# Performance work log

Measured on AMD Instinct MI355X. Metric: run time of the kernel, lower is better.

Reference implementation:

```python
import jax, jax.numpy as jnp
import numpy as np

B, L, D, NH, V, T, CYC = 16, 512, 512, 8, 8000, 17, 2
HD = D // NH


def _attn(q, kv, qw, qb, kw, kb, vw, vb, ow, ob):
    # q: [N, Lq, D], kv: [N, Lk, D]; weights stored [in, out] (= torch W.T)
    N, Lq, _ = q.shape
    Lk = kv.shape[1]
    Q = (q @ qw + qb).reshape(N, Lq, NH, HD)
    K = (kv @ kw + kb).reshape(N, Lk, NH, HD)
    Vv = (kv @ vw + vb).reshape(N, Lk, NH, HD)
    scores = jnp.einsum('nqhd,nkhd->nhqk', Q, K) / np.float32(np.sqrt(HD))
    probs = jax.nn.softmax(scores, axis=-1)
    ctx = jnp.einsum('nhqk,nkhd->nqhd', probs, Vv).reshape(N, Lq, D)
    return ctx @ ow + ob


def _ln(x, w, b, eps=1e-12):
    u = x.mean(-1, keepdims=True)
    s = ((x - u) ** 2).mean(-1, keepdims=True)
    return w * (x - u) / jnp.sqrt(s + eps) + b


def setup_inputs() -> dict:
    key = jax.random.key(0)
    ks = jax.random.split(key, 32)
    p = {}
    p['tokens'] = jax.random.randint(ks[0], (B, L, 1), 0, V)
    p['masks'] = jnp.ones((B, L), dtype=jnp.int64)
    p['heads'] = jax.random.randint(ks[1], (B, L), 0, 2)
    p['tails'] = jax.random.randint(ks[2], (B, L), 0, 2)
    p['char_emb'] = jax.random.normal(ks[3], (V, D), jnp.float32) * 0.02
    i = 4
    for pre in ('sat', 'rel'):
        for nm in ('q', 'k', 'v', 'o'):
            p[f'{pre}_{nm}w'] = jax.random.normal(ks[i], (D, D), jnp.float32) * 0.02
            p[f'{pre}_{nm}b'] = jnp.zeros((D,), jnp.float32)
            i += 1
    p['ln_sat_w'] = jnp.ones((D,), jnp.float32)
    p['ln_sat_b'] = jnp.zeros((D,), jnp.float32)
    p['ln_rel_w'] = jnp.ones((D,), jnp.float32)
    p['ln_rel_b'] = jnp.zeros((D,), jnp.float32)
    p['ofc_w'] = jax.random.normal(ks[i], (D, T), jnp.float32) * 0.02
    p['ofc_b'] = jnp.zeros((T,), jnp.float32)
    return p


def reference(tokens, masks, heads, tails, char_emb,
              sat_qw, sat_qb, sat_kw, sat_kb, sat_vw, sat_vb, sat_ow, sat_ob,
              rel_qw, rel_qb, rel_kw, rel_kb, rel_vw, rel_vb, rel_ow, rel_ob,
              ln_sat_w, ln_sat_b, ln_rel_w, ln_rel_b, ofc_w, ofc_b):
    e = char_emb[tokens[:, :, 0]]  # [B, L, D]
    h = e
    s = e.mean(axis=1)  # relay token [B, D] (avg_pool2d over seq)
    for _ in range(CYC):
        # backward cycle_shift in the source is a correct roll-by-(-1)
        h_last = jnp.roll(h, -1, axis=1)
        # forward cycle_shift in the source is sequential in-place: result[:,0]=h[:,-1],
        # result[:,i>=1]=h[:,0] (the write at i=0 propagates). Reproduced faithfully.
        h_next = jnp.concatenate(
            [h[:, -1:, :], jnp.broadcast_to(h[:, :1, :], (B, L - 1, D))], axis=1)
        sm = jnp.broadcast_to(s[:, None, :], (B, L, D))
        c = jnp.stack([h_last, h, h_next, e, sm], axis=2).reshape(B * L, 5, D)
        hq = h.reshape(B * L, 1, D)
        a = _attn(hq, c, sat_qw, sat_qb, sat_kw, sat_kb, sat_vw, sat_vb, sat_ow, sat_ob)
        h = _ln(jax.nn.relu(a), ln_sat_w, ln_sat_b).reshape(B, L, D)
        mc = jnp.concatenate([s[:, None, :], h], axis=1)  # [B, L+1, D]
        r = _attn(s[:, None, :], mc, rel_qw, rel_qb, rel_kw, rel_kb, rel_vw, rel_vb, rel_ow, rel_ob)
        s = _ln(jax.nn.relu(r), ln_rel_w, ln_rel_b)[:, 0, :]
    logits = h @ ofc_w + ofc_b  # [B, L, T]
    return logits
```

## Files before the change

### kernel.cpp

```cpp
#include <hip/hip_runtime.h>
#include <hip/hip_bf16.h>

typedef __hip_bfloat16 bf16;

#define BB 16
#define LL 512
#define DD 512
#define NHH 8
#define HDD 64
#define TT 17
#define MM (BB*LL)
#define RCH 8
#define RCK 65

typedef __attribute__((ext_vector_type(8))) short bfrag;
typedef __attribute__((ext_vector_type(4))) float ffrag;
typedef __attribute__((ext_vector_type(8))) unsigned short us8;

struct Params {
  const int* tokens;
  const float* emb;
  const float *sat_qw, *sat_qb, *sat_kw, *sat_kb, *sat_vw, *sat_vb, *sat_ow, *sat_ob;
  const float *rel_qw, *rel_qb, *rel_kw, *rel_kb, *rel_vw, *rel_vb, *rel_ow, *rel_ob;
  const float *ln_sat_w, *ln_sat_b, *ln_rel_w, *ln_rel_b, *ofc_w, *ofc_b;
  bf16 *ebf, *qkv, *kvbuf, *KeVe, *qbuf, *ctxbf, *WtAll, *WtO, *WtLog;
  float *s, *KsVs, *qr, *Ksr, *Vsr, *mpart, *pws, *out;
};

static __device__ __forceinline__ void gld16(const void* g, void* l){
  __builtin_amdgcn_global_load_lds((const __attribute__((address_space(1))) void*)g,
                                   (__attribute__((address_space(3))) void*)l, 16, 0, 0);
}
static __device__ __forceinline__ float us2f(unsigned short u){
  unsigned int v = ((unsigned int)u) << 16;
  float f; __builtin_memcpy(&f, &v, 4); return f;
}
static __device__ __forceinline__ float hsum8(float v){
  v += __shfl_xor(v, 1); v += __shfl_xor(v, 2); v += __shfl_xor(v, 4);
  return v;
}

__global__ __launch_bounds__(256) void k_init(Params P){
  __shared__ __align__(16) char sm[8192];
  int u = blockIdx.x, t = threadIdx.x;
  if (u < 256){
    int* toks = (int*)sm;
    int b = u >> 4, lc = u & 15;
    if (t < 32) toks[t] = P.tokens[b*LL + lc*32 + t];
    __syncthreads();
    bf16* eb = P.ebf + ((size_t)b*LL + lc*32)*DD;
    for (int d = t; d < DD; d += 256){
      float acc = 0.f;
      #pragma unroll 4
      for (int l = 0; l < 32; l++){
        float v = P.emb[(size_t)toks[l]*DD + d];
        eb[(size_t)l*DD + d] = __float2bfloat16(v);
        acc += v;
      }
      P.mpart[(size_t)u*DD + d] = acc;
    }
    return;
  }
  int w = u - 256;
  int z = w >> 8, xy = w & 255;
  int tx = t & 31, ty = t >> 5;
  if (z == 6){
    int i = (xy << 8) + t;
    int row = i >> 9, k = i & 511;
    P.WtLog[i] = __float2bfloat16(row < TT ? P.ofc_w[(size_t)k*TT + row] : 0.f);
    return;
  }
  float (*tile)[33] = (float(*)[33])sm;
  const float* in = (z==0)?P.sat_qw:(z==1)?P.sat_kw:(z==2)?P.sat_vw:
                    (z==3)?P.rel_kw:(z==4)?P.rel_vw:P.sat_ow;
  bf16* out = (z<5) ? (P.WtAll + (size_t)z*512*512) : P.WtO;
  int bx = (xy & 15)*32, by = (xy >> 4)*32;
  #pragma unroll
  for (int j = 0; j < 32; j += 8)
    tile[ty + j][tx] = in[(size_t)(by + ty + j)*DD + bx + tx];
  __syncthreads();
  #pragma unroll
  for (int j = 0; j < 32; j += 8)
    out[(size_t)(bx + ty + j)*DD + by + tx] = __float2bfloat16(tile[tx][ty + j]);
}

__global__ __launch_bounds__(256) void k_mean2(Params P){
  int i = blockIdx.x*256 + threadIdx.x;
  int b = i >> 9, d = i & 511;
  float acc = 0.f;
  #pragma unroll
  for (int c = 0; c < 16; c++) acc += P.mpart[(size_t)(b*16 + c)*DD + d];
  P.s[i] = acc * (1.0f/LL);
}

__global__ __launch_bounds__(256)
void k_sproj(Params P,
             const float* W0, const float* W1, const float* W2, const float* W3,
             const float* W4,
             const float* bias0, const float* bias1, const float* bias2,
             const float* bias3, const float* bias4,
             float* O0, float* O1, float* O2, float* O3, float* O4,
             int ldc0, int ldc1, int ldc2, int ldc3, int ldc4){
  __shared__ float part[8][32][17];
  const float* A = P.s;
  int t = threadIdx.x;
  int n = t & 31, kg = t >> 5;
  int wi = blockIdx.x >> 4, ch = blockIdx.x & 15;
  const float* W  = (wi==0)?W0:(wi==1)?W1:(wi==2)?W2:(wi==3)?W3:W4;
  const float* bs = (wi==0)?bias0:(wi==1)?bias1:(wi==2)?bias2:(wi==3)?bias3:bias4;
  float* O  = (wi==0)?O0:(wi==1)?O1:(wi==2)?O2:(wi==3)?O3:O4;
  int ldc   = (wi==0)?ldc0:(wi==1)?ldc1:(wi==2)?ldc2:(wi==3)?ldc3:ldc4;
  int col = ch*32 + n;
  float acc[16];
  #pragma unroll
  for (int m = 0; m < 16; m++) acc[m] = 0.f;
  const float* Wp = W + (size_t)(kg*64)*512 + col;
  const float* Ap = A + kg*64;
  for (int k = 0; k < 64; k++){
    float w = Wp[(size_t)k*512];
    #pragma unroll
    for (int m = 0; m < 16; m++) acc[m] = fmaf(Ap[m*512 + k], w, acc[m]);
  }
  #pragma unroll
  for (int m = 0; m < 16; m++) part[kg][n][m] = acc[m];
  __syncthreads();
  for (int o = t; o < 512; o += 256){
    int m = o >> 5, nn = o & 31;
    float v = 0.f;
    #pragma unroll
    for (int g = 0; g < 8; g++) v += part[g][nn][m];
    O[(size_t)m*ldc + ch*32 + nn] = v + bs[ch*32 + nn];
  }
}

__global__ __launch_bounds__(256)
void k_gemm(Params P, const bf16* __restrict__ A, const bf16* __restrict__ Wt,
            const float* b0, const float* b1, const float* b2, const float* b3,
            const float* b4,
            bf16* D0, int ld0, bf16* D1, int ld1, int split){
  const int K = 512;
  __shared__ bf16 As[128*32];
  __shared__ bf16 Bs[128*32];
  int t = threadIdx.x;
  int wave = t >> 6, lane = t & 63;
  int id = blockIdx.x;
  int bm = (((id & 7) << 3) | ((id >> 3) & 7)) * 128;
  int bn = (id >> 6) * 128;
  int wm = (wave & 1) * 64, wn = (wave >> 1) * 64;
  ffrag acc[4][4];
  #pragma unroll
  for (int i = 0; i < 4; i++)
    #pragma unroll
    for (int j = 0; j < 4; j++) acc[i][j] = (ffrag){0.f,0.f,0.f,0.f};

  int srow = t >> 2;
  int scol = ((((t & 3) - ((t >> 3) & 3)) & 3)) * 8;
  const bf16* gA = A  + (size_t)(bm + srow)*K + scol;
  const bf16* gB = Wt + (size_t)(bn + srow)*K + scol;
  char* lA = (char*)As + 16*t;
  char* lB = (char*)Bs + 16*t;
  int q = lane >> 4, r = lane & 15;
  int cs = (((q + (r >> 1)) & 3)) * 8;

  for (int k0 = 0; k0 < K; k0 += 32){
    gld16(gA + k0,          lA);
    gld16(gA + 64*K + k0,   lA + 4096);
    gld16(gB + k0,          lB);
    gld16(gB + 64*K + k0,   lB + 4096);
    __syncthreads();
    bfrag af[4], bfv[4];
    #pragma unroll
    for (int i = 0; i < 4; i++){
      af[i]  = *(const bfrag*)(As + (wm + i*16 + r)*32 + cs);
      bfv[i] = *(const bfrag*)(Bs + (wn + i*16 + r)*32 + cs);
    }
    #pragma unroll
    for (int i = 0; i < 4; i++)
      #pragma unroll
      for (int j = 0; j < 4; j++)
        acc[i][j] = __builtin_amdgcn_mfma_f32_16x16x32_bf16(af[i], bfv[j], acc[i][j], 0, 0, 0);
    __syncthreads();
  }
  #pragma unroll
  for (int i = 0; i < 4; i++){
    #pragma unroll
    for (int j = 0; j < 4; j++){
      int row = bm + wm + i*16 + q*4;
      int col = bn + wn + j*16 + r;
      const float* bp = (col < 512) ? b0 : (col < 1024) ? b1 :
                        (col < 1536) ? b2 : (col < 2048) ? b3 : b4;
      float bias = bp[col & 511];
      bf16* D; int ld;
      if (col < split){ D = D0 + (size_t)row*ld0 + col;         ld = ld0; }
      else            { D = D1 + (size_t)row*ld1 + (col-split); ld = ld1; }
      #pragma unroll
      for (int g = 0; g < 4; g++)
        D[(size_t)g*ld] = __float2bfloat16(acc[i][j][g] + bias);
    }
  }
}

__global__ __launch_bounds__(256) void k_logits(Params P){
  const int K = 512;
  __shared__ bf16 As[128*32];
  __shared__ bf16 Bs[128*32];
  int t = threadIdx.x;
  int wave = t >> 6, lane = t & 63;
  int bm = blockIdx.x * 128;
  int wm = (wave & 1) * 64, wn = (wave >> 1) * 64;
  ffrag acc[4][2];
  #pragma unroll
  for (int i = 0; i < 4; i++){ acc[i][0] = (ffrag){0,0,0,0}; acc[i][1] = (ffrag){0,0,0,0}; }
  int srow = t >> 2;
  int scol = ((((t & 3) - ((t >> 3) & 3)) & 3)) * 8;
  const bf16* gA = P.ebf + (size_t)(bm + srow)*K + scol;
  const bf16* gB = P.WtLog + (size_t)srow*K + scol;
  char* lA = (char*)As + 16*t;
  char* lB = (char*)Bs + 16*t;
  int q = lane >> 4, r = lane & 15;
  int cs = (((q + (r >> 1)) & 3)) * 8;

  for (int k0 = 0; k0 < K; k0 += 32){
    gld16(gA + k0,          lA);
    gld16(gA + 64*K + k0,   lA + 4096);
    gld16(gB + k0,          lB);
    gld16(gB + 64*K + k0,   lB + 4096);
    __syncthreads();
    if (wn == 0){
      bfrag bf0 = *(const bfrag*)(Bs + (r)*32 + cs);
      bfrag bf1 = *(const bfrag*)(Bs + (16 + r)*32 + cs);
      #pragma unroll
      for (int i = 0; i < 4; i++){
        bfrag af = *(const bfrag*)(As + (wm + i*16 + r)*32 + cs);
        acc[i][0] = __builtin_amdgcn_mfma_f32_16x16x32_bf16(af, bf0, acc[i][0], 0, 0, 0);
        acc[i][1] = __builtin_amdgcn_mfma_f32_16x16x32_bf16(af, bf1, acc[i][1], 0, 0, 0);
      }
    }
    __syncthreads();
  }
  if (wn == 0){
    #pragma unroll
    for (int i = 0; i < 4; i++)
      #pragma unroll
      for (int j = 0; j < 2; j++){
        int row = bm + wm + i*16 + q*4;
        int col = j*16 + r;
        if (col < TT){
          float bv = P.ofc_b[col];
          #pragma unroll
          for (int g = 0; g < 4; g++)
            P.out[(size_t)(row + g)*TT + col] = acc[i][j][g] + bv;
        }
      }
  }
}

__global__ __launch_bounds__(256)
void k_sat(Params P, const bf16* qp, int sq, const bf16* kp, const bf16* vp, int skv){
  int tok = blockIdx.x*4 + (threadIdx.x >> 6);
  int l = threadIdx.x & 63;
  int b = tok >> 9, li = tok & 511;
  int off = l*8;
  int t0 = (b << 9) | ((li + 1) & 511);
  int t2 = (b << 9) | (li == 0 ? 511 : 0);
  float qf[8];
  { us8 q8 = *(const us8*)(qp + (size_t)tok*sq + off);
    #pragma unroll
    for (int g = 0; g < 8; g++) qf[g] = us2f(q8[g]); }
  float sc[5];
  int rows[3] = {t0, tok, t2};
  #pragma unroll
  for (int j = 0; j < 3; j++){
    us8 k8 = *(const us8*)(kp + (size_t)rows[j]*skv + off);
    float a = 0.f;
    #pragma unroll
    for (int g = 0; g < 8; g++) a += qf[g]*us2f(k8[g]);
    sc[j] = hsum8(a) * 0.125f;
  }
  { us8 k8 = *(const us8*)(P.KeVe + (size_t)tok*1024 + off);
    float a = 0.f;
    #pragma unroll
    for (int g = 0; g < 8; g++) a += qf[g]*us2f(k8[g]);
    sc[3] = hsum8(a) * 0.125f; }
  { const float* ks = P.KsVs + (size_t)b*1024 + off;
    float4 f0 = *(const float4*)ks, f1 = *(const float4*)(ks + 4);
    float a = qf[0]*f0.x + qf[1]*f0.y + qf[2]*f0.z + qf[3]*f0.w
            + qf[4]*f1.x + qf[5]*f1.y + qf[6]*f1.z + qf[7]*f1.w;
    sc[4] = hsum8(a) * 0.125f; }
  float m = fmaxf(fmaxf(fmaxf(sc[0],sc[1]), fmaxf(sc[2],sc[3])), sc[4]);
  float pr[5], den = 0.f;
  #pragma unroll
  for (int j = 0; j < 5; j++){ pr[j] = __expf(sc[j]-m); den += pr[j]; }
  float inv = 1.0f/den;
  float o[8];
  #pragma unroll
  for (int g = 0; g < 8; g++) o[g] = 0.f;
  #pragma unroll
  for (int j = 0; j < 3; j++){
    us8 v8 = *(const us8*)(vp + (size_t)rows[j]*skv + off);
    #pragma unroll
    for (int g = 0; g < 8; g++) o[g] += pr[j]*us2f(v8[g]);
  }
  { us8 v8 = *(const us8*)(P.KeVe + (size_t)tok*1024 + 512 + off);
    #pragma unroll
    for (int g = 0; g < 8; g++) o[g] += pr[3]*us2f(v8[g]); }
  { const float* vs = P.KsVs + (size_t)b*1024 + 512 + off;
    float4 f0 = *(const float4*)vs, f1 = *(const float4*)(vs + 4);
    o[0] += pr[4]*f0.x; o[1] += pr[4]*f0.y; o[2] += pr[4]*f0.z; o[3] += pr[4]*f0.w;
    o[4] += pr[4]*f1.x; o[5] += pr[4]*f1.y; o[6] += pr[4]*f1.z; o[7] += pr[4]*f1.w; }
  bf16 ob[8];
  #pragma unroll
  for (int g = 0; g < 8; g++) ob[g] = __float2bfloat16(o[g]*inv);
  *(us8*)(P.ctxbf + (size_t)tok*DD + off) = *(const us8*)ob;
}

__global__ __launch_bounds__(256) void k_ln(Params P, const bf16* X, bf16* Y){
  int row = blockIdx.x*4 + (threadIdx.x >> 6);
  int lane = threadIdx.x & 63;
  int off = lane*8;
  us8 x8 = *(const us8*)(X + (size_t)row*DD + off);
  float v[8], sum = 0.f;
  #pragma unroll
  for (int g = 0; g < 8; g++){ v[g] = fmaxf(us2f(x8[g]), 0.f); sum += v[g]; }
  #pragma unroll
  for (int o = 32; o; o >>= 1) sum += __shfl_xor(sum, o);
  float u = sum * (1.0f/DD);
  float d[8], var = 0.f;
  #pragma unroll
  for (int g = 0; g < 8; g++){ d[g] = v[g] - u; var += d[g]*d[g]; }
  #pragma unroll
  for (int o = 32; o; o >>= 1) var += __shfl_xor(var, o);
  float inv = rsqrtf(var * (1.0f/DD) + 1e-12f);
  bf16 ob[8];
  #pragma unroll
  for (int g = 0; g < 8; g++)
    ob[g] = __float2bfloat16(P.ln_sat_w[off+g]*d[g]*inv + P.ln_sat_b[off+g]);
  *(us8*)(Y + (size_t)row*DD + off) = *(const us8*)ob;
}

__global__ __launch_bounds__(256) void k_relp(Params P){
  __shared__ __align__(16) char sm[4096];
  int u = blockIdx.x, t = threadIdx.x;
  int ch = u & 7, hh = (u >> 3) & 7, b = u >> 6;
  float* qs   = (float*)sm;
  float* sc   = (float*)(sm + 256);
  float* red  = (float*)(sm + 1024);
  float (*part)[64] = (float(*)[64])(sm + 2048);
  int base = hh * HDD;
  int j0 = ch * RCK;
  int nk = min(513 - j0, RCK);
  if (t < 64) qs[t] = P.qr[(size_t)b*DD + base + t];
  __syncthreads();
  if (t < nk){
    int j = j0 + t;
    float a = 0.f;
    if (j == 0){
      const float* kr = P.Ksr + (size_t)b*DD + base;
      #pragma unroll
      for (int d = 0; d < 64; d += 4){
        float4 k4 = *(const float4*)(kr + d);
        float4 q4 = *(const float4*)(qs + d);
        a += q4.x*k4.x + q4.y*k4.y + q4.z*k4.z + q4.w*k4.w;
      }
    } else {
      const bf16* kr = P.kvbuf + ((size_t)b*LL + j - 1)*1024 + base;
      #pragma unroll
      for (int d = 0; d < 64; d += 8){
        us8 k8 = *(const us8*)(kr + d);
        #pragma unroll
        for (int g = 0; g < 8; g++) a += qs[d+g] * us2f(k8[g]);
      }
    }
    sc[t] = a * 0.125f;
  }
  __syncthreads();
  red[t] = (t < nk) ? sc[t] : -1e30f; __syncthreads();
  for (int st = 128; st; st >>= 1){ if (t < st) red[t] = fmaxf(red[t], red[t+st]); __syncthreads(); }
  float m = red[0]; __syncthreads();
  if (t < nk) sc[t] = __expf(sc[t] - m);
  __syncthreads();
  red[t] = (t < nk) ? sc[t] : 0.f; __syncthreads();
  for (int st = 128; st; st >>= 1){ if (t < st) red[t] += red[t+st]; __syncthreads(); }
  float l = red[0];
  int d = t & 63, c2 = t >> 6;
  float a = 0.f;
  for (int j = c2; j < nk; j += 4){
    int gj = j0 + j;
    float vv = (gj == 0) ? P.Vsr[(size_t)b*DD + base + d]
                         : __bfloat162float(P.kvbuf[((size_t)b*LL + gj - 1)*1024 + 512 + base + d]);
    a += sc[j] * vv;
  }
  part[c2][d] = a; __syncthreads();
  float* o = P.pws + (((size_t)(b*NHH + hh))*RCH + ch) * 66;
  if (t < 64) o[t] = part[0][t] + part[1][t] + part[2][t] + part[3][t];
  else if (t == 64) o[64] = m;
  else if (t == 65) o[65] = l;
}

__global__ __launch_bounds__(256) void k_reltail(Params P){
  __shared__ __align__(16) char sm[4096];
  int b = blockIdx.x, t = threadIdx.x;
  float* crs = (float*)sm;
  float* red = (float*)(sm + 2048);
  for (int o = t; o < 512; o += 256){
    int hh = o >> 6, d = o & 63;
    const float* p = P.pws + ((size_t)(b*NHH + hh))*RCH*66;
    float M = -1e30f;
    #pragma unroll
    for (int c = 0; c < RCH; c++) M = fmaxf(M, p[c*66 + 64]);
    float den = 0.f, acc = 0.f;
    #pragma unroll
    for (int c = 0; c < RCH; c++){
      float w = __expf(p[c*66 + 64] - M);
      den += w * p[c*66 + 65];
      acc += w * p[c*66 + d];
    }
    crs[o] = acc / den;
  }
  __syncthreads();
  int n0 = t, n1 = t + 256;
  float a0 = P.rel_ob[n0], a1 = P.rel_ob[n1];
  for (int k = 0; k < 512; k++){
    float c = crs[k];
    a0 = fmaf(c, P.rel_ow[(size_t)k*512 + n0], a0);
    a1 = fmaf(c, P.rel_ow[(size_t)k*512 + n1], a1);
  }
  float v0 = fmaxf(a0, 0.f), v1 = fmaxf(a1, 0.f);
  red[t] = v0 + v1; __syncthreads();
  for (int st = 128; st; st >>= 1){ if (t < st) red[t] += red[t+st]; __syncthreads(); }
  float u = red[0] * (1.0f/DD); __syncthreads();
  float d0 = v0 - u, d1 = v1 - u;
  red[t] = d0*d0 + d1*d1; __syncthreads();
  for (int st = 128; st; st >>= 1){ if (t < st) red[t] += red[t+st]; __syncthreads(); }
  float inv = rsqrtf(red[0] * (1.0f/DD) + 1e-12f);
  P.s[(size_t)b*DD + n0] = P.ln_rel_w[n0]*d0*inv + P.ln_rel_b[n0];
  P.s[(size_t)b*DD + n1] = P.ln_rel_w[n1]*d1*inv + P.ln_rel_b[n1];
}

extern "C" void kernel_launch(void* const* d_in, const int* in_sizes, int n_in,
                              void* d_out, int out_size, void* d_ws, size_t ws_size,
                              hipStream_t stream) {
  Params P;
  P.tokens  = (const int*)  d_in[0];
  P.emb     = (const float*)d_in[4];
  P.sat_qw  = (const float*)d_in[5];  P.sat_qb = (const float*)d_in[6];
  P.sat_kw  = (const float*)d_in[7];  P.sat_kb = (const float*)d_in[8];
  P.sat_vw  = (const float*)d_in[9];  P.sat_vb = (const float*)d_in[10];
  P.sat_ow  = (const float*)d_in[11]; P.sat_ob = (const float*)d_in[12];
  P.rel_qw  = (const float*)d_in[13]; P.rel_qb = (const float*)d_in[14];
  P.rel_kw  = (const float*)d_in[15]; P.rel_kb = (const float*)d_in[16];
  P.rel_vw  = (const float*)d_in[17]; P.rel_vb = (const float*)d_in[18];
  P.rel_ow  = (const float*)d_in[19]; P.rel_ob = (const float*)d_in[20];
  P.ln_sat_w= (const float*)d_in[21]; P.ln_sat_b= (const float*)d_in[22];
  P.ln_rel_w= (const float*)d_in[23]; P.ln_rel_b= (const float*)d_in[24];
  P.ofc_w   = (const float*)d_in[25]; P.ofc_b  = (const float*)d_in[26];

  char* p = (char*)d_ws;
  auto alloc = [&](size_t bytes) -> char* {
    char* r = p; p += (bytes + 255) & ~(size_t)255; return r;
  };
  const size_t BIGH = (size_t)MM*DD*2;
  P.ebf   = (bf16*) alloc(BIGH);
  P.qkv   = (bf16*) alloc(3*BIGH);
  P.kvbuf = (bf16*) alloc(2*BIGH);
  P.KeVe  = (bf16*) alloc(2*BIGH);
  P.qbuf  = (bf16*) alloc(BIGH);
  P.ctxbf = (bf16*) alloc(BIGH);
  P.WtAll = (bf16*) alloc((size_t)2560*512*2);
  P.WtO   = (bf16*) alloc((size_t)512*512*2);
  P.WtLog = (bf16*) alloc((size_t)128*512*2);
  P.s     = (float*)alloc(BB*DD*4);
  P.KsVs  = (float*)alloc(BB*1024*4);
  P.qr    = (float*)alloc(BB*DD*4);
  P.Ksr   = (float*)alloc(BB*DD*4);
  P.Vsr   = (float*)alloc(BB*DD*4);
  P.mpart = (float*)alloc((size_t)256*DD*4);
  P.pws   = (float*)alloc((size_t)BB*NHH*RCH*66*4);
  P.out   = (float*)d_out;

  bf16* hbf  = P.ebf;
  bf16* aout = P.qkv;

  k_init<<<2048, 256, 0, stream>>>(P);
  k_mean2<<<32, 256, 0, stream>>>(P);
  k_sproj<<<80, 256, 0, stream>>>(P,
      P.sat_kw, P.sat_vw, P.rel_qw, P.rel_kw, P.rel_vw,
      P.sat_kb, P.sat_vb, P.rel_qb, P.rel_kb, P.rel_vb,
      P.KsVs, P.KsVs + 512, P.qr, P.Ksr, P.Vsr,
      1024, 1024, 512, 512, 512);
  k_gemm<<<768, 256, 0, stream>>>(P, P.ebf, P.WtAll,
      P.sat_qb, P.sat_kb, P.sat_vb, P.sat_vb, P.sat_vb, P.qbuf, 512, P.KeVe, 1024, 512);
  k_sat<<<MM/4, 256, 0, stream>>>(P, P.qbuf, 512, P.KeVe, P.KeVe + 512, 1024);
  k_gemm<<<256, 256, 0, stream>>>(P, P.ctxbf, P.WtO,
      P.sat_ob, P.sat_ob, P.sat_ob, P.sat_ob, P.sat_ob, aout, 512, aout, 512, 512);
  k_ln<<<MM/4, 256, 0, stream>>>(P, aout, hbf);
  k_gemm<<<1280, 256, 0, stream>>>(P, hbf, P.WtAll,
      P.sat_qb, P.sat_kb, P.sat_vb, P.rel_kb, P.rel_vb, P.qkv, 1536, P.kvbuf, 1024, 1536);
  k_relp<<<BB*NHH*RCH, 256, 0, stream>>>(P);
  k_reltail<<<BB, 256, 0, stream>>>(P);
  k_sproj<<<32, 256, 0, stream>>>(P,
      P.sat_kw, P.sat_vw, P.sat_vw, P.sat_vw, P.sat_vw,
      P.sat_kb, P.sat_vb, P.sat_vb, P.sat_vb, P.sat_vb,
      P.KsVs, P.KsVs + 512, P.Vsr, P.Vsr, P.Vsr,
      1024, 1024, 512, 512, 512);
  k_sat<<<MM/4, 256, 0, stream>>>(P, P.qkv, 1536, P.qkv + 512, P.qkv + 1024, 1536);
  k_gemm<<<256, 256, 0, stream>>>(P, P.ctxbf, P.WtO,
      P.sat_ob, P.sat_ob, P.sat_ob, P.sat_ob, P.sat_ob, aout, 512, aout, 512, 512);
  k_ln<<<MM/4, 256, 0, stream>>>(P, aout, hbf);
  k_logits<<<64, 256, 0, stream>>>(P);
}
```

Baseline: 335.3 us.

## Merge sproj into QKV gemm launch and split reltail across more blocks

```diff
diff --git a/kernel.cpp b/kernel.cpp
--- a/kernel.cpp
+++ b/kernel.cpp
@@ -93,19 +93,15 @@
   P.s[i] = acc * (1.0f/LL);
 }
 
-__global__ __launch_bounds__(256)
-void k_sproj(Params P,
-             const float* W0, const float* W1, const float* W2, const float* W3,
-             const float* W4,
-             const float* bias0, const float* bias1, const float* bias2,
-             const float* bias3, const float* bias4,
-             float* O0, float* O1, float* O2, float* O3, float* O4,
-             int ldc0, int ldc1, int ldc2, int ldc3, int ldc4){
-  __shared__ float part[8][32][17];
-  const float* A = P.s;
-  int t = threadIdx.x;
+static __device__ void sproj_unit(int u, int t, char* sm, const float* A,
+    const float* W0, const float* W1, const float* W2, const float* W3, const float* W4,
+    const float* bias0, const float* bias1, const float* bias2, const float* bias3,
+    const float* bias4,
+    float* O0, float* O1, float* O2, float* O3, float* O4,
+    int ldc0, int ldc1, int ldc2, int ldc3, int ldc4){
+  float (*part)[32][17] = (float(*)[32][17])sm;
   int n = t & 31, kg = t >> 5;
-  int wi = blockIdx.x >> 4, ch = blockIdx.x & 15;
+  int wi = u >> 4, ch = u & 15;
   const float* W  = (wi==0)?W0:(wi==1)?W1:(wi==2)?W2:(wi==3)?W3:W4;
   const float* bs = (wi==0)?bias0:(wi==1)?bias1:(wi==2)?bias2:(wi==3)?bias3:bias4;
   float* O  = (wi==0)?O0:(wi==1)?O1:(wi==2)?O2:(wi==3)?O3:O4;
@@ -133,17 +129,14 @@
   }
 }
 
-__global__ __launch_bounds__(256)
-void k_gemm(Params P, const bf16* __restrict__ A, const bf16* __restrict__ Wt,
-            const float* b0, const float* b1, const float* b2, const float* b3,
-            const float* b4,
-            bf16* D0, int ld0, bf16* D1, int ld1, int split){
+static __device__ void gemm_unit(int id, int t, char* sm,
+    const bf16* __restrict__ A, const bf16* __restrict__ Wt,
+    const float* b0, const float* b1, const float* b2, const float* b3, const float* b4,
+    bf16* D0, int ld0, bf16* D1, int ld1, int split){
   const int K = 512;
-  __shared__ bf16 As[128*32];
-  __shared__ bf16 Bs[128*32];
-  int t = threadIdx.x;
+  bf16* As = (bf16*)sm;
+  bf16* Bs = (bf16*)(sm + 8192);
   int wave = t >> 6, lane = t & 63;
-  int id = blockIdx.x;
   int bm = (((id & 7) << 3) | ((id >> 3) & 7)) * 128;
   int bn = (id >> 6) * 128;
   int wm = (wave & 1) * 64, wn = (wave >> 1) * 64;
@@ -198,6 +191,37 @@
         D[(size_t)g*ld] = __float2bfloat16(acc[i][j][g] + bias);
     }
   }
+}
+
+__global__ __launch_bounds__(256) void k_qkvsp(Params P){
+  __shared__ __align__(16) char sm[17408];
+  int u = blockIdx.x, t = threadIdx.x;
+  if (u < 768)
+    gemm_unit(u, t, sm, P.ebf, P.WtAll,
+              P.sat_qb, P.sat_kb, P.sat_vb, P.sat_vb, P.sat_vb,
+              P.qbuf, 512, P.KeVe, 1024, 512);
+  else
+    sproj_unit(u - 768, t, sm, P.s,
+               P.sat_kw, P.sat_vw, P.rel_qw, P.rel_kw, P.rel_vw,
+               P.sat_kb, P.sat_vb, P.rel_qb, P.rel_kb, P.rel_vb,
+               P.KsVs, P.KsVs + 512, P.qr, P.Ksr, P.Vsr,
+               1024, 1024, 512, 512, 512);
+}
+
+__global__ __launch_bounds__(256) void k_gemm(Params P, const bf16* A, const bf16* Wt,
+    const float* b0, const float* b1, const float* b2, const float* b3, const float* b4,
+    bf16* D0, int ld0, bf16* D1, int ld1, int split){
+  __shared__ __align__(16) char sm[16384];
+  gemm_unit(blockIdx.x, threadIdx.x, sm, A, Wt, b0, b1, b2, b3, b4, D0, ld0, D1, ld1, split);
+}
+
+__global__ __launch_bounds__(256) void k_sproj(Params P){
+  __shared__ __align__(16) char sm[17408];
+  sproj_unit(blockIdx.x, threadIdx.x, sm, P.s,
+             P.sat_kw, P.sat_vw, P.sat_vw, P.sat_vw, P.sat_vw,
+             P.sat_kb, P.sat_vb, P.sat_vb, P.sat_vb, P.sat_vb,
+             P.KsVs, P.KsVs + 512, P.Vsr, P.Vsr, P.Vsr,
+             1024, 1024, 512, 512, 512);
 }
 
 __global__ __launch_bounds__(256) void k_logits(Params P){
@@ -397,11 +421,11 @@
   else if (t == 65) o[65] = l;
 }
 
-__global__ __launch_bounds__(256) void k_reltail(Params P){
-  __shared__ __align__(16) char sm[4096];
-  int b = blockIdx.x, t = threadIdx.x;
-  float* crs = (float*)sm;
-  float* red = (float*)(sm + 2048);
+__global__ __launch_bounds__(256) void k_reltail2(Params P){
+  __shared__ float crs[512];
+  __shared__ float part[8][33];
+  int b = blockIdx.x >> 4, ch = blockIdx.x & 15;
+  int t = threadIdx.x;
   for (int o = t; o < 512; o += 256){
     int hh = o >> 6, d = o & 63;
     const float* p = P.pws + ((size_t)(b*NHH + hh))*RCH*66;
@@ -418,23 +442,44 @@
     crs[o] = acc / den;
   }
   __syncthreads();
-  int n0 = t, n1 = t + 256;
-  float a0 = P.rel_ob[n0], a1 = P.rel_ob[n1];
-  for (int k = 0; k < 512; k++){
-    float c = crs[k];
-    a0 = fmaf(c, P.rel_ow[(size_t)k*512 + n0], a0);
-    a1 = fmaf(c, P.rel_ow[(size_t)k*512 + n1], a1);
-  }
-  float v0 = fmaxf(a0, 0.f), v1 = fmaxf(a1, 0.f);
-  red[t] = v0 + v1; __syncthreads();
-  for (int st = 128; st; st >>= 1){ if (t < st) red[t] += red[t+st]; __syncthreads(); }
-  float u = red[0] * (1.0f/DD); __syncthreads();
-  float d0 = v0 - u, d1 = v1 - u;
-  red[t] = d0*d0 + d1*d1; __syncthreads();
-  for (int st = 128; st; st >>= 1){ if (t < st) red[t] += red[t+st]; __syncthreads(); }
-  float inv = rsqrtf(red[0] * (1.0f/DD) + 1e-12f);
-  P.s[(size_t)b*DD + n0] = P.ln_rel_w[n0]*d0*inv + P.ln_rel_b[n0];
-  P.s[(size_t)b*DD + n1] = P.ln_rel_w[n1]*d1*inv + P.ln_rel_b[n1];
+  int n = t & 31, kg = t >> 5;
+  int col = ch*32 + n;
+  const float* Wp = P.rel_ow + (size_t)(kg*64)*512 + col;
+  const float* cp = crs + kg*64;
+  float a = 0.f;
+  for (int k = 0; k < 64; k++) a = fmaf(cp[k], Wp[(size_t)k*512], a);
+  part[kg][n] = a;
+  __syncthreads();
+  if (t < 32){
+    float v = P.rel_ob[ch*32 + t];
+    #pragma unroll
+    for (int g = 0; g < 8; g++) v += part[g][t];
+    P.qr[(size_t)b*DD + ch*32 + t] = v;
+  }
+}
+
+__global__ __launch_bounds__(256) void k_lnrel(Params P){
+  int row = blockIdx.x*4 + (threadIdx.x >> 6);
+  int lane = threadIdx.x & 63;
+  int off = lane*8;
+  const float* x = P.qr + (size_t)row*DD + off;
+  float4 f0 = *(const float4*)x, f1 = *(const float4*)(x + 4);
+  float v[8] = {f0.x, f0.y, f0.z, f0.w, f1.x, f1.y, f1.z, f1.w};
+  float sum = 0.f;
+  #pragma unroll
+  for (int g = 0; g < 8; g++){ v[g] = fmaxf(v[g], 0.f); sum += v[g]; }
+  #pragma unroll
+  for (int o = 32; o; o >>= 1) sum += __shfl_xor(sum, o);
+  float u = sum * (1.0f/DD);
+  float d[8], var = 0.f;
+  #pragma unroll
+  for (int g = 0; g < 8; g++){ d[g] = v[g] - u; var += d[g]*d[g]; }
+  #pragma unroll
+  for (int o = 32; o; o >>= 1) var += __shfl_xor(var, o);
+  float inv = rsqrtf(var * (1.0f/DD) + 1e-12f);
+  #pragma unroll
+  for (int g = 0; g < 8; g++)
+    P.s[(size_t)row*DD + off + g] = P.ln_rel_w[off+g]*d[g]*inv + P.ln_rel_b[off+g];
 }
 
 extern "C" void kernel_launch(void* const* d_in, const int* in_sizes, int n_in,
@@ -483,13 +528,7 @@
 
   k_init<<<2048, 256, 0, stream>>>(P);
   k_mean2<<<32, 256, 0, stream>>>(P);
-  k_sproj<<<80, 256, 0, stream>>>(P,
-      P.sat_kw, P.sat_vw, P.rel_qw, P.rel_kw, P.rel_vw,
-      P.sat_kb, P.sat_vb, P.rel_qb, P.rel_kb, P.rel_vb,
-      P.KsVs, P.KsVs + 512, P.qr, P.Ksr, P.Vsr,
-      1024, 1024, 512, 512, 512);
-  k_gemm<<<768, 256, 0, stream>>>(P, P.ebf, P.WtAll,
-      P.sat_qb, P.sat_kb, P.sat_vb, P.sat_vb, P.sat_vb, P.qbuf, 512, P.KeVe, 1024, 512);
+  k_qkvsp<<<848, 256, 0, stream>>>(P);
   k_sat<<<MM/4, 256, 0, stream>>>(P, P.qbuf, 512, P.KeVe, P.KeVe + 512, 1024);
   k_gemm<<<256, 256, 0, stream>>>(P, P.ctxbf, P.WtO,
       P.sat_ob, P.sat_ob, P.sat_ob, P.sat_ob, P.sat_ob, aout, 512, aout, 512, 512);
@@ -497,12 +536,9 @@
   k_gemm<<<1280, 256, 0, stream>>>(P, hbf, P.WtAll,
       P.sat_qb, P.sat_kb, P.sat_vb, P.rel_kb, P.rel_vb, P.qkv, 1536, P.kvbuf, 1024, 1536);
   k_relp<<<BB*NHH*RCH, 256, 0, stream>>>(P);
-  k_reltail<<<BB, 256, 0, stream>>>(P);
-  k_sproj<<<32, 256, 0, stream>>>(P,
-      P.sat_kw, P.sat_vw, P.sat_vw, P.sat_vw, P.sat_vw,
-      P.sat_kb, P.sat_vb, P.sat_vb, P.sat_vb, P.sat_vb,
-      P.KsVs, P.KsVs + 512, P.Vsr, P.Vsr, P.Vsr,
-      1024, 1024, 512, 512, 512);
+  k_reltail2<<<256, 256, 0, stream>>>(P);
+  k_lnrel<<<4, 256, 0, stream>>>(P);
+  k_sproj<<<32, 256, 0, stream>>>(P);
   k_sat<<<MM/4, 256, 0, stream>>>(P, P.qkv, 1536, P.qkv + 512, P.qkv + 1024, 1536);
   k_gemm<<<256, 256, 0, stream>>>(P, P.ctxbf, P.WtO,
       P.sat_ob, P.sat_ob, P.sat_ob, P.sat_ob, P.sat_ob, aout, 512, aout, 512, 512);
```

After: 359.6 us. 1.07x slower.
